# Kernel tuning notes

Hardware: AMD Instinct MI355X
Metric: run time of the kernel (lower is better)

Reference implementation:

```python
import jax, jax.numpy as jnp
import numpy as np

D = 512
N_WAY = 64
K_SHOT = 16
N_QUERY = 8192


def setup_inputs() -> dict:
    key = jax.random.key(0)
    k1, k2, k3, k4 = jax.random.split(key, 4)
    support = jax.random.normal(k1, (N_WAY * K_SHOT, D), dtype=jnp.float32)
    query = jax.random.normal(k2, (N_QUERY, D), dtype=jnp.float32)
    # nn.Linear(input_dim, input_dim) params (kaiming-uniform-ish scale)
    bound = 1.0 / np.sqrt(D)
    W = jax.random.uniform(k3, (D, D), minval=-bound, maxval=bound, dtype=jnp.float32)
    b = jax.random.uniform(k4, (D,), minval=-bound, maxval=bound, dtype=jnp.float32)
    return {"support": support, "query": query, "W": W, "b": b,
            "n_way": N_WAY, "k_shot": K_SHOT}


def reference(support, query, W, b, n_way, k_shot):
    # shared linear projection: x @ W^T + b (torch nn.Linear convention)
    support_emb = support @ W.T + b            # [n_way*k_shot, d]
    query_emb = query @ W.T + b                # [n_q, d]
    # class prototypes: mean over the k_shot axis
    prototypes = support_emb.reshape(n_way, k_shot, -1).mean(axis=1)  # [n_way, d]
    # pairwise squared euclidean distances (broadcast sub/square/sum,
    # same math as the torch euclidean_dist)
    diff = query_emb[:, None, :] - prototypes[None, :, :]  # [n_q, n_way, d]
    dists = jnp.sum(diff * diff, axis=-1)                  # [n_q, n_way]
    return dists
```

## Files before the change

### kernel.cpp

```cpp
#include <hip/hip_runtime.h>
#include <hip/hip_bf16.h>

#define D 512
#define NWAY 64
#define KSHOT 16
#define NQ 8192

typedef __bf16 bf16_t;
typedef __bf16 bf16x8_t __attribute__((ext_vector_type(8)));
typedef __bf16 bf16x4_t __attribute__((ext_vector_type(4)));
typedef float  f32x4    __attribute__((ext_vector_type(4)));

typedef __attribute__((address_space(1))) const void gv_t;
typedef __attribute__((address_space(3))) void lv_t;
__device__ __forceinline__ void ld16(const void* g, void* l) {
    __builtin_amdgcn_global_load_lds((gv_t*)g, (lv_t*)l, 16, 0, 0);
}


__global__ __launch_bounds__(256) void k_prep1(
    const float* __restrict__ sup, const float* __restrict__ W,
    const float* __restrict__ bias, float* __restrict__ Pg,
    bf16_t* __restrict__ Bsw)
{
    const int b = blockIdx.x, t = threadIdx.x;

    if (b < 256) {
        const int c = b >> 2, jq = b & 3;
        __shared__ __align__(16) float cm[D];
        {
            const int d = t * 2;
            float sx = 0.f, sy = 0.f;
#pragma unroll
            for (int j = 0; j < KSHOT; ++j) {
                float2 v = *(const float2*)(sup + (size_t)(c * KSHOT + j) * D + d);
                sx += v.x; sy += v.y;
            }
            cm[d] = sx * (1.0f / KSHOT); cm[d + 1] = sy * (1.0f / KSHOT);
        }
        __syncthreads();
        const int j = jq * 128 + (t >> 1);
        const int half = t & 1;
        const f32x4* wr = (const f32x4*)(W + (size_t)j * D + half * 256);
        const f32x4* cr = (const f32x4*)(cm + half * 256);
        float s = 0.f;
#pragma unroll 8
        for (int i = 0; i < 64; ++i) {
            f32x4 a = cr[i], wv = wr[i];
            s += a[0]*wv[0] + a[1]*wv[1] + a[2]*wv[2] + a[3]*wv[3];
        }
        s += __shfl_xor(s, 1);
        if (!half) Pg[(size_t)c * D + j] = s + bias[j];
        return;
    }

    {
        const int n = (b - 256) * 4 + (t >> 6);
        const int sl = t & 63;
        const f32x4* wp = (const f32x4*)(W + (size_t)n * D + sl * 8);
        f32x4 v0 = wp[0], v1 = wp[1];
        bf16x8_t hv = { (bf16_t)v0[0], (bf16_t)v0[1], (bf16_t)v0[2], (bf16_t)v0[3],
                        (bf16_t)v1[0], (bf16_t)v1[1], (bf16_t)v1[2], (bf16_t)v1[3] };
        const int ck = sl >> 3, s = sl & 7;
        *(bf16x8_t*)(Bsw + (size_t)ck * 36864 + n * 64 + ((s ^ (n & 7)) * 8)) = hv;
    }
}

__global__ __launch_bounds__(256) void k_prep2(
    const float* __restrict__ Pg, const float* __restrict__ W,
    const float* __restrict__ bias, bf16_t* __restrict__ Bsw,
    float* __restrict__ ph)
{
    __shared__ __align__(16) float Pl[D];
    __shared__ float sG[2][128];
    __shared__ float red[4];

    const int c = blockIdx.x >> 2, kc = blockIdx.x & 3;
    const int t = threadIdx.x;
    const int kl = t & 127, jh = t >> 7;
    const int k = kc * 128 + kl;

    ((float2*)Pl)[t] = ((const float2*)(Pg + (size_t)c * D))[t];
    __syncthreads();

    float g = 0.f;
    const float* wcol = W + (size_t)jh * 256 * D + k;
#pragma unroll 8
    for (int j = 0; j < 256; ++j)
        g += Pl[jh * 256 + j] * wcol[(size_t)j * D];
    sG[jh][kl] = g;

    if (kc == 0) {
        float v1 = Pl[t], v2 = Pl[t + 256];
        float pp = v1 * v1 - 2.0f * bias[t] * v1 + v2 * v2 - 2.0f * bias[t + 256] * v2;
#pragma unroll
        for (int off = 32; off; off >>= 1) pp += __shfl_xor(pp, off);
        if ((t & 63) == 0) red[t >> 6] = pp;
    }
    __syncthreads();

    if (jh == 0) {
        const float gt = sG[0][kl] + sG[1][kl];
        const int n = 512 + c;
        const int ck = k >> 6, s = (k >> 3) & 7, e = k & 7;
        Bsw[(size_t)ck * 36864 + n * 64 + ((s ^ (c & 7)) * 8) + e] = (bf16_t)gt;
    }
    if (kc == 0 && t == 0) ph[c] = red[0] + red[1] + red[2] + red[3];
}

__global__ __launch_bounds__(512, 2) void k_main(
    const float* __restrict__ query, const bf16_t* __restrict__ Bsw,
    const float* __restrict__ bias, const float* __restrict__ ph,
    float* __restrict__ out)
{
    __shared__ bf16_t Bb[2][36864];
    __shared__ bf16_t Ab[2][2048];
    __shared__ float qln[4][32];
    __shared__ float phs[NWAY];
    __shared__ float bs[576];

    const int t = threadIdx.x, bm = blockIdx.x;
    bs[t] = bias[t];
    if (t < NWAY) { bs[512 + t] = 0.f; phs[t] = ph[t]; }

    const int l = t & 63, w = t >> 6;
    const int wm = w & 1, wn = w >> 1;
    const int r15 = l & 15, quad = l >> 4;

    const int xt0 = ((quad ^ (r15 & 7)) * 8);
    const int xt1 = (((4 + quad) ^ (r15 & 7)) * 8);
    const int aoff = (wm * 16 + r15) * 64;
    const int boff = (wn * 144 + r15) * 64;
    const int wb = w * 4608 + l * 8;

    const int am = t >> 4;
    const int ac4 = t & 15;
    const int a_lds = am * 64 + (((ac4 >> 1) ^ (am & 7)) * 8) + (ac4 & 1) * 4;
    const float* aqp = query + (size_t)(bm * 32 + am) * D + ac4 * 4;

    bf16x4_t areg[8];
#pragma unroll
    for (int ck = 0; ck < 8; ++ck) {
        f32x4 v = *(const f32x4*)(aqp + ck * 64);
        areg[ck] = (bf16x4_t){ (bf16_t)v[0], (bf16_t)v[1], (bf16_t)v[2], (bf16_t)v[3] };
    }

    f32x4 acc[9];
#pragma unroll
    for (int i = 0; i < 9; ++i) acc[i] = (f32x4){0.f, 0.f, 0.f, 0.f};

    {
#pragma unroll
        for (int i = 0; i < 9; ++i)
            ld16(Bsw + wb + i * 512, &Bb[0][wb + i * 512]);
        *(bf16x4_t*)(&Ab[0][a_lds]) = areg[0];
    }
    __syncthreads();

#pragma unroll
    for (int ck = 0; ck < 8; ++ck) {
        const int cur = ck & 1;
        if (ck < 7) {
            const int nxt = cur ^ 1;
            const size_t sb = (size_t)(ck + 1) * 36864;
#pragma unroll
            for (int i = 0; i < 9; ++i)
                ld16(Bsw + sb + wb + i * 512, &Bb[nxt][wb + i * 512]);
            *(bf16x4_t*)(&Ab[nxt][a_lds]) = areg[ck + 1];
        }

        bf16x8_t a0 = *(const bf16x8_t*)(&Ab[cur][aoff + xt0]);
        bf16x8_t a1 = *(const bf16x8_t*)(&Ab[cur][aoff + xt1]);
#pragma unroll
        for (int tt = 0; tt < 9; ++tt) {
            bf16x8_t b0 = *(const bf16x8_t*)(&Bb[cur][boff + tt * 1024 + xt0]);
            bf16x8_t b1 = *(const bf16x8_t*)(&Bb[cur][boff + tt * 1024 + xt1]);
            acc[tt] = __builtin_amdgcn_mfma_f32_16x16x32_bf16(a0, b0, acc[tt], 0, 0, 0);
            acc[tt] = __builtin_amdgcn_mfma_f32_16x16x32_bf16(a1, b1, acc[tt], 0, 0, 0);
        }

        if (ck < 7) __syncthreads();
    }

    float qp[4] = {0.f, 0.f, 0.f, 0.f};
#pragma unroll
    for (int tt = 0; tt < 9; ++tt) {
        const int colbase = wn * 144 + tt * 16;
        const float m = (colbase < 512) ? 1.f : 0.f;
        const float bv = bs[colbase + r15];
#pragma unroll
        for (int reg = 0; reg < 4; ++reg) {
            float v = acc[tt][reg] + bv;
            qp[reg] += m * v * v;
        }
    }
#pragma unroll
    for (int reg = 0; reg < 4; ++reg) {
        float s = qp[reg];
        s += __shfl_xor(s, 1); s += __shfl_xor(s, 2);
        s += __shfl_xor(s, 4); s += __shfl_xor(s, 8);
        if (r15 == 0) qln[wn][wm * 16 + quad * 4 + reg] = s;
    }
    __syncthreads();

    if (wn == 3) {
#pragma unroll
        for (int reg = 0; reg < 4; ++reg) {
            const int row_local = quad * 4 + reg;
            const float qt = qln[0][wm * 16 + row_local] + qln[1][wm * 16 + row_local] +
                             qln[2][wm * 16 + row_local] + qln[3][wm * 16 + row_local];
            const int rowg = bm * 32 + wm * 16 + row_local;
#pragma unroll
            for (int tg = 0; tg < 4; ++tg) {
                const int c = tg * 16 + r15;
                out[(size_t)rowg * NWAY + c] = qt + phs[c] - 2.0f * acc[5 + tg][reg];
            }
        }
    }
}

extern "C" void kernel_launch(void* const* d_in, const int* in_sizes, int n_in,
                              void* d_out, int out_size, void* d_ws, size_t ws_size,
                              hipStream_t stream)
{
    const float* support = (const float*)d_in[0];
    const float* query   = (const float*)d_in[1];
    const float* W       = (const float*)d_in[2];
    const float* bias    = (const float*)d_in[3];
    float* out = (float*)d_out;

    char* ws = (char*)d_ws;
    bf16_t* Bsw = (bf16_t*)ws;
    float*  ph  = (float*)(ws + 589824);
    float*  Pg  = (float*)(ws + 589824 + 256);

    k_prep1<<<384, 256, 0, stream>>>(support, W, bias, Pg, Bsw);
    k_prep2<<<256, 256, 0, stream>>>(Pg, W, bias, Bsw, ph);
    k_main<<<256, 512, 0, stream>>>(query, Bsw, bias, ph, out);
}
```

Baseline: 110.6 us.

## Merge two prep kernels into one launch computing prototypes and projections per class

Fuses k_prep1 and k_prep2 into a single k_prep kernel. One 512-thread block per class computes the support mean, the prototype projection P = W·mean + b, the prototype norm term, and the W^T·P column. Extra blocks handle the bf16 swizzled conversion of W. This removes one kernel launch and the Pg round trip through global memory. In exchange it uses far fewer blocks for the serial dot-product work (64 blocks versus 256+256), so each thread runs longer 512-iteration loops with less parallelism.

```diff
diff --git a/kernel.cpp b/kernel.cpp
--- a/kernel.cpp
+++ b/kernel.cpp
@@ -18,94 +18,81 @@
 }
 
 
-__global__ __launch_bounds__(256) void k_prep1(
+__global__ __launch_bounds__(512) void k_prep(
     const float* __restrict__ sup, const float* __restrict__ W,
-    const float* __restrict__ bias, float* __restrict__ Pg,
-    bf16_t* __restrict__ Bsw)
-{
-    const int b = blockIdx.x, t = threadIdx.x;
-
-    if (b < 256) {
-        const int c = b >> 2, jq = b & 3;
-        __shared__ __align__(16) float cm[D];
-        {
-            const int d = t * 2;
-            float sx = 0.f, sy = 0.f;
-#pragma unroll
-            for (int j = 0; j < KSHOT; ++j) {
-                float2 v = *(const float2*)(sup + (size_t)(c * KSHOT + j) * D + d);
-                sx += v.x; sy += v.y;
-            }
-            cm[d] = sx * (1.0f / KSHOT); cm[d + 1] = sy * (1.0f / KSHOT);
-        }
-        __syncthreads();
-        const int j = jq * 128 + (t >> 1);
-        const int half = t & 1;
-        const f32x4* wr = (const f32x4*)(W + (size_t)j * D + half * 256);
-        const f32x4* cr = (const f32x4*)(cm + half * 256);
-        float s = 0.f;
-#pragma unroll 8
-        for (int i = 0; i < 64; ++i) {
-            f32x4 a = cr[i], wv = wr[i];
-            s += a[0]*wv[0] + a[1]*wv[1] + a[2]*wv[2] + a[3]*wv[3];
-        }
-        s += __shfl_xor(s, 1);
-        if (!half) Pg[(size_t)c * D + j] = s + bias[j];
-        return;
-    }
-
-    {
-        const int n = (b - 256) * 4 + (t >> 6);
-        const int sl = t & 63;
-        const f32x4* wp = (const f32x4*)(W + (size_t)n * D + sl * 8);
-        f32x4 v0 = wp[0], v1 = wp[1];
-        bf16x8_t hv = { (bf16_t)v0[0], (bf16_t)v0[1], (bf16_t)v0[2], (bf16_t)v0[3],
-                        (bf16_t)v1[0], (bf16_t)v1[1], (bf16_t)v1[2], (bf16_t)v1[3] };
-        const int ck = sl >> 3, s = sl & 7;
-        *(bf16x8_t*)(Bsw + (size_t)ck * 36864 + n * 64 + ((s ^ (n & 7)) * 8)) = hv;
-    }
-}
-
-__global__ __launch_bounds__(256) void k_prep2(
-    const float* __restrict__ Pg, const float* __restrict__ W,
     const float* __restrict__ bias, bf16_t* __restrict__ Bsw,
     float* __restrict__ ph)
 {
+    const int b = blockIdx.x, t = threadIdx.x;
+
+    if (b >= 64) {
+        const int n = (b - 64) * 4 + (t >> 7);
+        const int q = t & 127;
+        f32x4 v = *(const f32x4*)(W + (size_t)n * D + q * 4);
+        bf16x4_t hv = { (bf16_t)v[0], (bf16_t)v[1], (bf16_t)v[2], (bf16_t)v[3] };
+        const int seg = q >> 1;
+        const int ck = seg >> 3, ss = seg & 7;
+        *(bf16x4_t*)(Bsw + (size_t)ck * 36864 + n * 64 +
+                     ((ss ^ (n & 7)) * 8) + (q & 1) * 4) = hv;
+        return;
+    }
+
+    const int c = b;
+    __shared__ __align__(16) float cm[D];
     __shared__ __align__(16) float Pl[D];
-    __shared__ float sG[2][128];
-    __shared__ float red[4];
-
-    const int c = blockIdx.x >> 2, kc = blockIdx.x & 3;
-    const int t = threadIdx.x;
-    const int kl = t & 127, jh = t >> 7;
-    const int k = kc * 128 + kl;
-
-    ((float2*)Pl)[t] = ((const float2*)(Pg + (size_t)c * D))[t];
-    __syncthreads();
-
-    float g = 0.f;
-    const float* wcol = W + (size_t)jh * 256 * D + k;
+    __shared__ float red[8];
+
+    if (t < 256) {
+        const int d = t * 2;
+        float sx = 0.f, sy = 0.f;
+#pragma unroll
+        for (int j = 0; j < KSHOT; ++j) {
+            float2 v = *(const float2*)(sup + (size_t)(c * KSHOT + j) * D + d);
+            sx += v.x; sy += v.y;
+        }
+        cm[d] = sx * (1.0f / KSHOT); cm[d + 1] = sy * (1.0f / KSHOT);
+    }
+    __syncthreads();
+
+    {
+        const f32x4* wr = (const f32x4*)(W + (size_t)t * D);
+        const f32x4* cr = (const f32x4*)cm;
+        float s = 0.f;
 #pragma unroll 8
-    for (int j = 0; j < 256; ++j)
-        g += Pl[jh * 256 + j] * wcol[(size_t)j * D];
-    sG[jh][kl] = g;
-
-    if (kc == 0) {
-        float v1 = Pl[t], v2 = Pl[t + 256];
-        float pp = v1 * v1 - 2.0f * bias[t] * v1 + v2 * v2 - 2.0f * bias[t + 256] * v2;
+        for (int i = 0; i < 128; ++i) {
+            f32x4 a = cr[i], wv = wr[i];
+            s += a[0]*wv[0] + a[1]*wv[1] + a[2]*wv[2] + a[3]*wv[3];
+        }
+        Pl[t] = s + bias[t];
+    }
+    __syncthreads();
+
+    {
+        const float v = Pl[t];
+        float pp = v * v - 2.0f * bias[t] * v;
 #pragma unroll
         for (int off = 32; off; off >>= 1) pp += __shfl_xor(pp, off);
         if ((t & 63) == 0) red[t >> 6] = pp;
     }
-    __syncthreads();
-
-    if (jh == 0) {
-        const float gt = sG[0][kl] + sG[1][kl];
+
+    {
+        float g = 0.f;
+        const float* wc = W + t;
+#pragma unroll 16
+        for (int j = 0; j < 512; ++j)
+            g += Pl[j] * wc[(size_t)j * D];
         const int n = 512 + c;
-        const int ck = k >> 6, s = (k >> 3) & 7, e = k & 7;
-        Bsw[(size_t)ck * 36864 + n * 64 + ((s ^ (c & 7)) * 8) + e] = (bf16_t)gt;
-    }
-    if (kc == 0 && t == 0) ph[c] = red[0] + red[1] + red[2] + red[3];
+        const int ck = t >> 6, s = (t >> 3) & 7, e = t & 7;
+        Bsw[(size_t)ck * 36864 + n * 64 + ((s ^ (c & 7)) * 8) + e] = (bf16_t)g;
+    }
+
+    __syncthreads();
+    if (t == 0) {
+        float s = 0.f;
+#pragma unroll
+        for (int i = 0; i < 8; ++i) s += red[i];
+        ph[c] = s;
+    }
 }
 
 __global__ __launch_bounds__(512, 2) void k_main(
@@ -120,7 +107,7 @@
     __shared__ float bs[576];
 
     const int t = threadIdx.x, bm = blockIdx.x;
-    bs[t] = bias[t];
+    bs[t] = bias[t < 512 ? t : 511];
     if (t < NWAY) { bs[512 + t] = 0.f; phs[t] = ph[t]; }
 
     const int l = t & 63, w = t >> 6;
@@ -232,9 +219,7 @@
     char* ws = (char*)d_ws;
     bf16_t* Bsw = (bf16_t*)ws;
     float*  ph  = (float*)(ws + 589824);
-    float*  Pg  = (float*)(ws + 589824 + 256);
-
-    k_prep1<<<384, 256, 0, stream>>>(support, W, bias, Pg, Bsw);
-    k_prep2<<<256, 256, 0, stream>>>(Pg, W, bias, Bsw, ph);
+
+    k_prep<<<192, 512, 0, stream>>>(support, W, bias, Bsw, ph);
     k_main<<<256, 512, 0, stream>>>(query, Bsw, bias, ph, out);
 }
```

After: 127.4 us. +15.2%, slower.

## Split K across wave pairs so each B fragment feeds two row tiles

Applied to the files above, without the earlier changes.

Each wave pair previously split the 32 query rows (16 each) and walked the whole 64-wide K chunk. Now each wave covers all 32 rows over half of the K chunk, so a single B fragment load feeds two MFMAs (one per row tile) and B LDS reads per wave are halved. The two partial accumulators are then reduced through LDS, reusing the B buffer, before the norm and distance epilogue. In exchange, accumulator registers double and an extra LDS exchange plus barrier is added at the end.

```diff
diff --git a/kernel.cpp b/kernel.cpp
--- a/kernel.cpp
+++ b/kernel.cpp
@@ -113,8 +113,8 @@
     const float* __restrict__ bias, const float* __restrict__ ph,
     float* __restrict__ out)
 {
-    __shared__ bf16_t Bb[2][36864];
-    __shared__ bf16_t Ab[2][2048];
+    __shared__ __align__(16) bf16_t Bb[2][36864];
+    __shared__ __align__(16) bf16_t Ab[2][2048];
     __shared__ float qln[4][32];
     __shared__ float phs[NWAY];
     __shared__ float bs[576];
@@ -127,9 +127,9 @@
     const int wm = w & 1, wn = w >> 1;
     const int r15 = l & 15, quad = l >> 4;
 
-    const int xt0 = ((quad ^ (r15 & 7)) * 8);
-    const int xt1 = (((4 + quad) ^ (r15 & 7)) * 8);
-    const int aoff = (wm * 16 + r15) * 64;
+    const int xth = (((wm * 4 + quad) ^ (r15 & 7)) * 8);
+    const int aoff0 = r15 * 64;
+    const int aoff1 = (16 + r15) * 64;
     const int boff = (wn * 144 + r15) * 64;
     const int wb = w * 4608 + l * 8;
 
@@ -145,9 +145,11 @@
         areg[ck] = (bf16x4_t){ (bf16_t)v[0], (bf16_t)v[1], (bf16_t)v[2], (bf16_t)v[3] };
     }
 
-    f32x4 acc[9];
-#pragma unroll
-    for (int i = 0; i < 9; ++i) acc[i] = (f32x4){0.f, 0.f, 0.f, 0.f};
+    f32x4 acc[2][9];
+#pragma unroll
+    for (int rg = 0; rg < 2; ++rg)
+#pragma unroll
+        for (int i = 0; i < 9; ++i) acc[rg][i] = (f32x4){0.f, 0.f, 0.f, 0.f};
 
     {
 #pragma unroll
@@ -169,51 +171,72 @@
             *(bf16x4_t*)(&Ab[nxt][a_lds]) = areg[ck + 1];
         }
 
-        bf16x8_t a0 = *(const bf16x8_t*)(&Ab[cur][aoff + xt0]);
-        bf16x8_t a1 = *(const bf16x8_t*)(&Ab[cur][aoff + xt1]);
+        bf16x8_t a0 = *(const bf16x8_t*)(&Ab[cur][aoff0 + xth]);
+        bf16x8_t a1 = *(const bf16x8_t*)(&Ab[cur][aoff1 + xth]);
 #pragma unroll
         for (int tt = 0; tt < 9; ++tt) {
-            bf16x8_t b0 = *(const bf16x8_t*)(&Bb[cur][boff + tt * 1024 + xt0]);
-            bf16x8_t b1 = *(const bf16x8_t*)(&Bb[cur][boff + tt * 1024 + xt1]);
-            acc[tt] = __builtin_amdgcn_mfma_f32_16x16x32_bf16(a0, b0, acc[tt], 0, 0, 0);
-            acc[tt] = __builtin_amdgcn_mfma_f32_16x16x32_bf16(a1, b1, acc[tt], 0, 0, 0);
+            bf16x8_t bv = *(const bf16x8_t*)(&Bb[cur][boff + tt * 1024 + xth]);
+            acc[0][tt] = __builtin_amdgcn_mfma_f32_16x16x32_bf16(a0, bv, acc[0][tt], 0, 0, 0);
+            acc[1][tt] = __builtin_amdgcn_mfma_f32_16x16x32_bf16(a1, bv, acc[1][tt], 0, 0, 0);
         }
 
         if (ck < 7) __syncthreads();
     }
 
-    float qp[4] = {0.f, 0.f, 0.f, 0.f};
-#pragma unroll
-    for (int tt = 0; tt < 9; ++tt) {
-        const int colbase = wn * 144 + tt * 16;
-        const float m = (colbase < 512) ? 1.f : 0.f;
-        const float bv = bs[colbase + r15];
+    f32x4* exf = (f32x4*)&Bb[0][0];
+    if (wm == 1) {
+#pragma unroll
+        for (int rg = 0; rg < 2; ++rg)
+#pragma unroll
+            for (int tt = 0; tt < 9; ++tt)
+                exf[((wn * 18 + rg * 9 + tt) << 6) + l] = acc[rg][tt];
+    }
+    __syncthreads();
+    if (wm == 0) {
+#pragma unroll
+        for (int rg = 0; rg < 2; ++rg)
+#pragma unroll
+            for (int tt = 0; tt < 9; ++tt)
+                acc[rg][tt] = acc[rg][tt] + exf[((wn * 18 + rg * 9 + tt) << 6) + l];
+
+#pragma unroll
+        for (int rg = 0; rg < 2; ++rg) {
+            float qp[4] = {0.f, 0.f, 0.f, 0.f};
+#pragma unroll
+            for (int tt = 0; tt < 9; ++tt) {
+                const int colbase = wn * 144 + tt * 16;
+                const float m = (colbase < 512) ? 1.f : 0.f;
+                const float bv = bs[colbase + r15];
+#pragma unroll
+                for (int reg = 0; reg < 4; ++reg) {
+                    float v = acc[rg][tt][reg] + bv;
+                    qp[reg] += m * v * v;
+                }
+            }
+#pragma unroll
+            for (int reg = 0; reg < 4; ++reg) {
+                float s = qp[reg];
+                s += __shfl_xor(s, 1); s += __shfl_xor(s, 2);
+                s += __shfl_xor(s, 4); s += __shfl_xor(s, 8);
+                if (r15 == 0) qln[wn][rg * 16 + quad * 4 + reg] = s;
+            }
+        }
+    }
+    __syncthreads();
+
+    if (wm == 0 && wn == 3) {
+#pragma unroll
+        for (int rg = 0; rg < 2; ++rg)
 #pragma unroll
         for (int reg = 0; reg < 4; ++reg) {
-            float v = acc[tt][reg] + bv;
-            qp[reg] += m * v * v;
-        }
-    }
-#pragma unroll
-    for (int reg = 0; reg < 4; ++reg) {
-        float s = qp[reg];
-        s += __shfl_xor(s, 1); s += __shfl_xor(s, 2);
-        s += __shfl_xor(s, 4); s += __shfl_xor(s, 8);
-        if (r15 == 0) qln[wn][wm * 16 + quad * 4 + reg] = s;
-    }
-    __syncthreads();
-
-    if (wn == 3) {
-#pragma unroll
-        for (int reg = 0; reg < 4; ++reg) {
-            const int row_local = quad * 4 + reg;
-            const float qt = qln[0][wm * 16 + row_local] + qln[1][wm * 16 + row_local] +
-                             qln[2][wm * 16 + row_local] + qln[3][wm * 16 + row_local];
-            const int rowg = bm * 32 + wm * 16 + row_local;
+            const int row_local = rg * 16 + quad * 4 + reg;
+            const float qt = qln[0][row_local] + qln[1][row_local] +
+                             qln[2][row_local] + qln[3][row_local];
+            const int rowg = bm * 32 + row_local;
 #pragma unroll
             for (int tg = 0; tg < 4; ++tg) {
                 const int c = tg * 16 + r15;
-                out[(size_t)rowg * NWAY + c] = qt + phs[c] - 2.0f * acc[5 + tg][reg];
+                out[(size_t)rowg * NWAY + c] = qt + phs[c] - 2.0f * acc[rg][5 + tg][reg];
             }
         }
     }
```

After: 112.8 us. 1.02x slower.

## Fuse three kernels into one cooperative launch with grid-wide syncs

Applied to the files above, without the earlier changes.

Merges the two prep kernels and the main GEMM kernel into a single cooperative kernel of 256 blocks, using grid.sync between the prototype projection, the W-transpose-times-prototype stage, and the main MFMA loop. The query rows are loaded before the prep work so their global latency overlaps it, and prep work is redistributed across 512-thread blocks. This is meant to remove two kernel launch gaps and tail effects. In exchange it adds two grid-wide barriers and requires all 256 blocks to be co-resident, and the prep stages now run on fewer blocks than before.

```diff
diff --git a/kernel.cpp b/kernel.cpp
--- a/kernel.cpp
+++ b/kernel.cpp
@@ -1,5 +1,8 @@
 #include <hip/hip_runtime.h>
 #include <hip/hip_bf16.h>
+#include <hip/hip_cooperative_groups.h>
+
+namespace cg = cooperative_groups;
 
 #define D 512
 #define NWAY 64
@@ -18,108 +21,113 @@
 }
 
 
-__global__ __launch_bounds__(256) void k_prep1(
-    const float* __restrict__ sup, const float* __restrict__ W,
-    const float* __restrict__ bias, float* __restrict__ Pg,
-    bf16_t* __restrict__ Bsw)
+__global__ __launch_bounds__(512, 2) void k_fused(
+    const float* __restrict__ sup, const float* __restrict__ query,
+    const float* __restrict__ W, const float* __restrict__ bias,
+    bf16_t* __restrict__ Bsw, float* __restrict__ ph,
+    float* __restrict__ Pg, float* __restrict__ out)
 {
-    const int b = blockIdx.x, t = threadIdx.x;
-
-    if (b < 256) {
-        const int c = b >> 2, jq = b & 3;
-        __shared__ __align__(16) float cm[D];
-        {
-            const int d = t * 2;
-            float sx = 0.f, sy = 0.f;
-#pragma unroll
-            for (int j = 0; j < KSHOT; ++j) {
-                float2 v = *(const float2*)(sup + (size_t)(c * KSHOT + j) * D + d);
-                sx += v.x; sy += v.y;
-            }
-            cm[d] = sx * (1.0f / KSHOT); cm[d + 1] = sy * (1.0f / KSHOT);
-        }
-        __syncthreads();
-        const int j = jq * 128 + (t >> 1);
-        const int half = t & 1;
-        const f32x4* wr = (const f32x4*)(W + (size_t)j * D + half * 256);
-        const f32x4* cr = (const f32x4*)(cm + half * 256);
-        float s = 0.f;
-#pragma unroll 8
-        for (int i = 0; i < 64; ++i) {
-            f32x4 a = cr[i], wv = wr[i];
-            s += a[0]*wv[0] + a[1]*wv[1] + a[2]*wv[2] + a[3]*wv[3];
-        }
-        s += __shfl_xor(s, 1);
-        if (!half) Pg[(size_t)c * D + j] = s + bias[j];
-        return;
-    }
-
-    {
-        const int n = (b - 256) * 4 + (t >> 6);
-        const int sl = t & 63;
-        const f32x4* wp = (const f32x4*)(W + (size_t)n * D + sl * 8);
-        f32x4 v0 = wp[0], v1 = wp[1];
-        bf16x8_t hv = { (bf16_t)v0[0], (bf16_t)v0[1], (bf16_t)v0[2], (bf16_t)v0[3],
-                        (bf16_t)v1[0], (bf16_t)v1[1], (bf16_t)v1[2], (bf16_t)v1[3] };
-        const int ck = sl >> 3, s = sl & 7;
-        *(bf16x8_t*)(Bsw + (size_t)ck * 36864 + n * 64 + ((s ^ (n & 7)) * 8)) = hv;
-    }
-}
-
-__global__ __launch_bounds__(256) void k_prep2(
-    const float* __restrict__ Pg, const float* __restrict__ W,
-    const float* __restrict__ bias, bf16_t* __restrict__ Bsw,
-    float* __restrict__ ph)
-{
-    __shared__ __align__(16) float Pl[D];
-    __shared__ float sG[2][128];
-    __shared__ float red[4];
-
-    const int c = blockIdx.x >> 2, kc = blockIdx.x & 3;
-    const int t = threadIdx.x;
-    const int kl = t & 127, jh = t >> 7;
-    const int k = kc * 128 + kl;
-
-    ((float2*)Pl)[t] = ((const float2*)(Pg + (size_t)c * D))[t];
-    __syncthreads();
-
-    float g = 0.f;
-    const float* wcol = W + (size_t)jh * 256 * D + k;
-#pragma unroll 8
-    for (int j = 0; j < 256; ++j)
-        g += Pl[jh * 256 + j] * wcol[(size_t)j * D];
-    sG[jh][kl] = g;
-
-    if (kc == 0) {
-        float v1 = Pl[t], v2 = Pl[t + 256];
-        float pp = v1 * v1 - 2.0f * bias[t] * v1 + v2 * v2 - 2.0f * bias[t + 256] * v2;
-#pragma unroll
-        for (int off = 32; off; off >>= 1) pp += __shfl_xor(pp, off);
-        if ((t & 63) == 0) red[t >> 6] = pp;
-    }
-    __syncthreads();
-
-    if (jh == 0) {
-        const float gt = sG[0][kl] + sG[1][kl];
-        const int n = 512 + c;
-        const int ck = k >> 6, s = (k >> 3) & 7, e = k & 7;
-        Bsw[(size_t)ck * 36864 + n * 64 + ((s ^ (c & 7)) * 8) + e] = (bf16_t)gt;
-    }
-    if (kc == 0 && t == 0) ph[c] = red[0] + red[1] + red[2] + red[3];
-}
-
-__global__ __launch_bounds__(512, 2) void k_main(
-    const float* __restrict__ query, const bf16_t* __restrict__ Bsw,
-    const float* __restrict__ bias, const float* __restrict__ ph,
-    float* __restrict__ out)
-{
-    __shared__ bf16_t Bb[2][36864];
-    __shared__ bf16_t Ab[2][2048];
+    __shared__ __align__(16) bf16_t Bb[2][36864];
+    __shared__ __align__(16) bf16_t Ab[2][2048];
     __shared__ float qln[4][32];
     __shared__ float phs[NWAY];
     __shared__ float bs[576];
 
     const int t = threadIdx.x, bm = blockIdx.x;
+    cg::grid_group grid = cg::this_grid();
+
+    const int am = t >> 4;
+    const int ac4 = t & 15;
+    const int a_lds = am * 64 + (((ac4 >> 1) ^ (am & 7)) * 8) + (ac4 & 1) * 4;
+    const float* aqp = query + (size_t)(bm * 32 + am) * D + ac4 * 4;
+    f32x4 av[8];
+#pragma unroll
+    for (int ck = 0; ck < 8; ++ck) av[ck] = *(const f32x4*)(aqp + ck * 64);
+
+    {
+        const int c = bm >> 2, jq4 = bm & 3;
+        float* cm = (float*)&Bb[0][0];
+        {
+            float s = 0.f;
+            const float* sp = sup + (size_t)c * KSHOT * D + t;
+#pragma unroll
+            for (int j = 0; j < KSHOT; ++j) s += sp[(size_t)j * D];
+            cm[t] = s * (1.0f / KSHOT);
+        }
+        __syncthreads();
+        {
+            const int j = jq4 * 128 + (t >> 2), qtr = t & 3;
+            const f32x4* wr = (const f32x4*)(W + (size_t)j * D + qtr * 128);
+            const f32x4* cr = (const f32x4*)(cm + qtr * 128);
+            float ps = 0.f;
+#pragma unroll 8
+            for (int i = 0; i < 32; ++i) {
+                f32x4 a = cr[i], wv = wr[i];
+                ps += a[0]*wv[0] + a[1]*wv[1] + a[2]*wv[2] + a[3]*wv[3];
+            }
+            ps += __shfl_xor(ps, 1); ps += __shfl_xor(ps, 2);
+            if (qtr == 0) Pg[(size_t)c * D + j] = ps + bias[j];
+        }
+        if (t < 128) {
+            const int n = bm * 2 + (t >> 6);
+            const int sl = t & 63;
+            const f32x4* wp = (const f32x4*)(W + (size_t)n * D + sl * 8);
+            f32x4 v0 = wp[0], v1 = wp[1];
+            bf16x8_t hv = { (bf16_t)v0[0], (bf16_t)v0[1], (bf16_t)v0[2], (bf16_t)v0[3],
+                            (bf16_t)v1[0], (bf16_t)v1[1], (bf16_t)v1[2], (bf16_t)v1[3] };
+            const int ckk = sl >> 3, ss = sl & 7;
+            *(bf16x8_t*)(Bsw + (size_t)ckk * 36864 + n * 64 + ((ss ^ (n & 7)) * 8)) = hv;
+        }
+    }
+
+    bf16x4_t areg[8];
+#pragma unroll
+    for (int ck = 0; ck < 8; ++ck)
+        areg[ck] = (bf16x4_t){ (bf16_t)av[ck][0], (bf16_t)av[ck][1],
+                               (bf16_t)av[ck][2], (bf16_t)av[ck][3] };
+
+    __threadfence();
+    grid.sync();
+
+    {
+        const int c = bm >> 2, kc = bm & 3;
+        float* Pl  = (float*)&Bb[0][0];
+        float* sGm = (float*)&Bb[0][4096];
+        float* red = (float*)&Bb[0][8192];
+        Pl[t] = Pg[(size_t)c * D + t];
+        __syncthreads();
+
+        const int kl = t & 127, jq = t >> 7;
+        const int k = kc * 128 + kl;
+        float g = 0.f;
+        const float* wcol = W + (size_t)jq * 128 * D + k;
+#pragma unroll 8
+        for (int j = 0; j < 128; ++j)
+            g += Pl[jq * 128 + j] * wcol[(size_t)j * D];
+        sGm[jq * 128 + kl] = g;
+
+        if (kc == 0 && t < 256) {
+            float v1 = Pl[t], v2 = Pl[t + 256];
+            float pp = v1*v1 - 2.0f*bias[t]*v1 + v2*v2 - 2.0f*bias[t+256]*v2;
+#pragma unroll
+            for (int off = 32; off; off >>= 1) pp += __shfl_xor(pp, off);
+            if ((t & 63) == 0) red[t >> 6] = pp;
+        }
+        __syncthreads();
+
+        if (t < 128) {
+            const float gt = sGm[t] + sGm[128 + t] + sGm[256 + t] + sGm[384 + t];
+            const int k2 = kc * 128 + t;
+            const int n = 512 + c;
+            const int ckk = k2 >> 6, ss = (k2 >> 3) & 7, e = k2 & 7;
+            Bsw[(size_t)ckk * 36864 + n * 64 + ((ss ^ (c & 7)) * 8) + e] = (bf16_t)gt;
+        }
+        if (kc == 0 && t == 0) ph[c] = red[0] + red[1] + red[2] + red[3];
+    }
+
+    __threadfence();
+    grid.sync();
+
     bs[t] = bias[t];
     if (t < NWAY) { bs[512 + t] = 0.f; phs[t] = ph[t]; }
 
@@ -132,18 +140,6 @@
     const int aoff = (wm * 16 + r15) * 64;
     const int boff = (wn * 144 + r15) * 64;
     const int wb = w * 4608 + l * 8;
-
-    const int am = t >> 4;
-    const int ac4 = t & 15;
-    const int a_lds = am * 64 + (((ac4 >> 1) ^ (am & 7)) * 8) + (ac4 & 1) * 4;
-    const float* aqp = query + (size_t)(bm * 32 + am) * D + ac4 * 4;
-
-    bf16x4_t areg[8];
-#pragma unroll
-    for (int ck = 0; ck < 8; ++ck) {
-        f32x4 v = *(const f32x4*)(aqp + ck * 64);
-        areg[ck] = (bf16x4_t){ (bf16_t)v[0], (bf16_t)v[1], (bf16_t)v[2], (bf16_t)v[3] };
-    }
 
     f32x4 acc[9];
 #pragma unroll
@@ -234,7 +230,8 @@
     float*  ph  = (float*)(ws + 589824);
     float*  Pg  = (float*)(ws + 589824 + 256);
 
-    k_prep1<<<384, 256, 0, stream>>>(support, W, bias, Pg, Bsw);
-    k_prep2<<<256, 256, 0, stream>>>(Pg, W, bias, Bsw, ph);
-    k_main<<<256, 512, 0, stream>>>(query, Bsw, bias, ph, out);
+    void* kargs[] = { (void*)&support, (void*)&query, (void*)&W, (void*)&bias,
+                      (void*)&Bsw, (void*)&ph, (void*)&Pg, (void*)&out };
+    hipLaunchCooperativeKernel((const void*)k_fused, dim3(256), dim3(512),
+                               kargs, 0, stream);
 }
```

Result: slower. 261.0 us (+136.0%).
